# Optimization experiments

Measured on AMD Instinct MI355X. Metric: run time of the kernel, lower is better.

The kernel has to match this reference:

```python
import jax, jax.numpy as jnp
import numpy as np

# Config matching init_kwargs: layer_nb=1 -> stride 16, image 608x608 -> 38x38 grid
B, CIN, H, W = 32, 512, 38, 38
NA, NC = 3, 80
STRIDE = 16.0
ANCHORS = np.array([[30.0, 61.0], [62.0, 45.0], [59.0, 119.0]], dtype=np.float32)


def setup_inputs() -> dict:
    key = jax.random.key(0)
    k1, k2, k3 = jax.random.split(key, 3)
    xin = jax.random.normal(k1, (B, CIN, H, W), dtype=jnp.float32)
    # 1x1 conv weight stored as (out_ch, in_ch); out_ch = NA*(NC+5) = 255
    conv_w = jax.random.normal(k2, (NA * (NC + 5), CIN), dtype=jnp.float32) * 0.02
    conv_b = jax.random.normal(k3, (NA * (NC + 5),), dtype=jnp.float32) * 0.01
    return {"xin": xin, "conv_w": conv_w, "conv_b": conv_b}


def reference(xin, conv_w, conv_b):
    # 1x1 conv == channel GEMM; fuse the NCHW->NHWC permute into the einsum
    fm = jnp.einsum('bchw,oc->bhwo', xin, conv_w) + conv_b  # [B,H,W,255]
    fm = fm.reshape(B, H, W, NA, NC + 5)
    tx, ty, tw, th = fm[..., 0], fm[..., 1], fm[..., 2], fm[..., 3]
    # grid offsets (precomputed via broadcasting instead of per-call numpy rebuild)
    x_off = jnp.arange(W, dtype=fm.dtype)[None, None, :, None]   # broadcast over B,H,NA
    y_off = jnp.arange(H, dtype=fm.dtype)[None, :, None, None]   # broadcast over B,W,NA
    anchors = jnp.asarray(ANCHORS, dtype=fm.dtype)               # [NA,2]
    bx = (jax.nn.sigmoid(tx) + x_off) * STRIDE
    by = (jax.nn.sigmoid(ty) + y_off) * STRIDE
    bw = jnp.exp(tw) * anchors[:, 0]
    bh = jnp.exp(th) * anchors[:, 1]
    boxes = jnp.stack([bx, by, bw, bh], axis=-1)                 # [B,H,W,NA,4]
    # concat decoded boxes with raw objectness + class logits -> [B,H,W,NA,85]
    return jnp.concatenate([boxes, fm[..., 4:]], axis=-1)
```

## Files before the change

kernel.cpp:

```cpp
#include <hip/hip_runtime.h>
#include <cstdint>
#include <cstddef>

#define CIN_K  512
#define WW_    38
#define BHW    1444
#define NOUT   255
#define MTOT   46208

#define BM     32
#define KCH    256
#define ROW_E  260
#define EP_DW  260

typedef __attribute__((ext_vector_type(8))) short  bf16x8;
typedef __attribute__((ext_vector_type(4))) float  floatx4;

static __device__ __forceinline__ unsigned f2bf(float f) {
    unsigned u = __builtin_bit_cast(unsigned, f);
    return (u + 0x7FFFu + ((u >> 16) & 1u)) >> 16;
}

__global__ void conv_w_to_bf16(const float* __restrict__ cw,
                               unsigned short* __restrict__ wb) {
    int tg   = blockIdx.x * 256 + threadIdx.x;
    int base = tg * 8;
    int n    = base >> 9;
    unsigned rr[4] = {0u, 0u, 0u, 0u};
    if (n < NOUT) {
        float4 v0 = *(const float4*)(cw + base);
        float4 v1 = *(const float4*)(cw + base + 4);
        rr[0] = f2bf(v0.x) | (f2bf(v0.y) << 16);
        rr[1] = f2bf(v0.z) | (f2bf(v0.w) << 16);
        rr[2] = f2bf(v1.x) | (f2bf(v1.y) << 16);
        rr[3] = f2bf(v1.z) | (f2bf(v1.w) << 16);
    }
    *(uint4*)(wb + base) = *(uint4*)rr;
}

__global__ __launch_bounds__(256, 6)
void yolo_head(const float* __restrict__ xin,
               const unsigned short* __restrict__ wb,
               const float* __restrict__ cb,
               float* __restrict__ out)
{
    __shared__ unsigned smem[BM * (ROW_E / 2)];
    unsigned short* As = (unsigned short*)smem;

    const int t    = threadIdx.x;
    const int w    = t >> 6;
    const int lane = t & 63;
    const int l15  = lane & 15;
    const int q    = lane >> 4;
    const int m0   = blockIdx.x * BM;

    const int mq4 = (t & 7) * 4;
    const int kq4 = (t >> 3) * 4;
    const int m4  = m0 + mq4;
    const int bi  = m4 / BHW;
    const int hw  = m4 - bi * BHW;
    const float* pb0 = xin + (size_t)bi * (CIN_K * BHW) + hw;

    floatx4 acc[2][4];
#pragma unroll
    for (int i = 0; i < 2; ++i)
#pragma unroll
        for (int j = 0; j < 4; ++j)
            acc[i][j] = (floatx4){0.f, 0.f, 0.f, 0.f};

    const unsigned short* pbw = wb + (size_t)(w * 64 + l15) * CIN_K + q * 8;

#pragma unroll
    for (int ck = 0; ck < 2; ++ck) {
        if (ck) __syncthreads();

#pragma unroll
        for (int it = 0; it < 2; ++it) {
            const int kl = it * 128 + kq4;
            alignas(16) float vv[4][4];
#pragma unroll
            for (int kk = 0; kk < 4; ++kk)
                *(float4*)&vv[kk][0] =
                    *(const float4*)(pb0 + (size_t)(ck * KCH + kl + kk) * BHW);
#pragma unroll
            for (int r = 0; r < 4; ++r) {
                unsigned lo = f2bf(vv[0][r]) | (f2bf(vv[1][r]) << 16);
                unsigned hi = f2bf(vv[2][r]) | (f2bf(vv[3][r]) << 16);
                uint2 pk = make_uint2(lo, hi);
                *(uint2*)(&As[(mq4 + r) * ROW_E + kl]) = pk;
            }
        }
        __syncthreads();

#pragma unroll
        for (int kc = 0; kc < 8; ++kc) {
            bf16x8 bfr[4], af[2];
#pragma unroll
            for (int j = 0; j < 4; ++j) {
                uint4 bv = *(const uint4*)(pbw + (size_t)j * 16 * CIN_K
                                           + ck * KCH + kc * 32);
                bfr[j] = __builtin_bit_cast(bf16x8, bv);
            }
#pragma unroll
            for (int i = 0; i < 2; ++i) {
                int4 av = *(const int4*)(&As[(i * 16 + l15) * ROW_E + kc * 32 + q * 8]);
                af[i] = __builtin_bit_cast(bf16x8, av);
            }
#pragma unroll
            for (int i = 0; i < 2; ++i)
#pragma unroll
                for (int j = 0; j < 4; ++j)
                    acc[i][j] = __builtin_amdgcn_mfma_f32_16x16x32_bf16(
                                    af[i], bfr[j], acc[i][j], 0, 0, 0);
        }
    }

#pragma unroll
    for (int j = 0; j < 4; ++j) {
        int   n    = w * 64 + j * 16 + l15;
        int   nc   = n < NOUT ? n : NOUT - 1;
        int   ai   = nc / 85;
        int   ji   = nc - ai * 85;
        float bias = cb[nc];
        float aw   = (ai == 0) ? 30.f : (ai == 1) ? 62.f : 59.f;
        float ah   = (ai == 0) ? 61.f : (ai == 1) ? 45.f : 119.f;
#pragma unroll
        for (int i = 0; i < 2; ++i)
#pragma unroll
            for (int r = 0; r < 4; ++r) {
                int   md  = m0 + i * 16 + q * 4 + r;
                int   rem = md % BHW;
                int   hh  = rem / WW_;
                float v   = acc[i][j][r] + bias;
                float res;
                if (ji == 0)      res = (1.f / (1.f + __expf(-v)) + (float)(rem - hh * WW_)) * 16.f;
                else if (ji == 1) res = (1.f / (1.f + __expf(-v)) + (float)hh) * 16.f;
                else if (ji == 2) res = __expf(v) * aw;
                else if (ji == 3) res = __expf(v) * ah;
                else              res = v;
                acc[i][j][r] = res;
            }
    }

    float* EP = (float*)smem;
#pragma unroll
    for (int p = 0; p < 2; ++p) {
        __syncthreads();
#pragma unroll
        for (int j = 0; j < 4; ++j)
#pragma unroll
            for (int r = 0; r < 4; ++r)
                EP[(q * 4 + r) * EP_DW + w * 64 + j * 16 + l15] = acc[p][j][r];
        __syncthreads();

        const float* EPb = (const float*)smem + (w * 4) * EP_DW;
        float*       ob  = out + (size_t)(m0 + p * 16 + w * 4) * NOUT;
#pragma unroll
        for (int s2 = 0; s2 < 4; ++s2) {
            int f4 = s2 * 64 + lane;
            if (f4 < 255) {
                int   f = f4 * 4;
                float vs[4];
#pragma unroll
                for (int e = 0; e < 4; ++e) {
                    int fe = f + e;
                    int mr = fe / NOUT;
                    int x  = fe - mr * NOUT;
                    vs[e]  = EPb[mr * EP_DW + x];
                }
                *(float4*)(ob + f) = make_float4(vs[0], vs[1], vs[2], vs[3]);
            }
        }
    }
}

extern "C" void kernel_launch(void* const* d_in, const int* in_sizes, int n_in,
                              void* d_out, int out_size, void* d_ws, size_t ws_size,
                              hipStream_t stream) {
    const float* xin = (const float*)d_in[0];
    const float* cw  = (const float*)d_in[1];
    const float* cb  = (const float*)d_in[2];
    float*       out = (float*)d_out;
    unsigned short* wb = (unsigned short*)d_ws;

    hipLaunchKernelGGL(conv_w_to_bf16, dim3(64), dim3(256), 0, stream, cw, wb);
    hipLaunchKernelGGL(yolo_head, dim3(MTOT / BM), dim3(256), 0, stream,
                       xin, wb, cb, out);
}
```

Measured before the change: 202.4 us.

## Prefetch second K-chunk into registers and remap blocks across XCDs

The kernel issues the global loads for the second 256-channel K chunk into registers before computing on the first chunk, so their latency overlaps the first chunk's MFMA loop. It also remaps block IDs so each XCD handles a contiguous range of M tiles, which is meant to improve L2 locality on the multi-XCD part. The occupancy hint drops from 6 to 4 waves per SIMD to make room for the extra prefetch registers. The trade-off is fewer resident workgroups available to hide memory latency.

```diff
diff --git a/kernel.cpp b/kernel.cpp
--- a/kernel.cpp
+++ b/kernel.cpp
@@ -38,7 +38,7 @@
     *(uint4*)(wb + base) = *(uint4*)rr;
 }
 
-__global__ __launch_bounds__(256, 6)
+__global__ __launch_bounds__(256, 4)
 void yolo_head(const float* __restrict__ xin,
                const unsigned short* __restrict__ wb,
                const float* __restrict__ cb,
@@ -52,7 +52,12 @@
     const int lane = t & 63;
     const int l15  = lane & 15;
     const int q    = lane >> 4;
-    const int m0   = blockIdx.x * BM;
+
+    const int orig = blockIdx.x;
+    const int xcd  = orig & 7;
+    const int rank = orig >> 3;
+    const int wgid = (xcd < 4 ? xcd * 181 : 724 + (xcd - 4) * 180) + rank;
+    const int m0   = wgid * BM;
 
     const int mq4 = (t & 7) * 4;
     const int kq4 = (t >> 3) * 4;
@@ -61,6 +66,30 @@
     const int hw  = m4 - bi * BHW;
     const float* pb0 = xin + (size_t)bi * (CIN_K * BHW) + hw;
 
+    alignas(16) float v0[2][4][4];
+#pragma unroll
+    for (int it = 0; it < 2; ++it)
+#pragma unroll
+        for (int kk = 0; kk < 4; ++kk)
+            *(float4*)&v0[it][kk][0] =
+                *(const float4*)(pb0 + (size_t)(it * 128 + kq4 + kk) * BHW);
+#pragma unroll
+    for (int it = 0; it < 2; ++it)
+#pragma unroll
+        for (int r = 0; r < 4; ++r) {
+            unsigned lo = f2bf(v0[it][0][r]) | (f2bf(v0[it][1][r]) << 16);
+            unsigned hi = f2bf(v0[it][2][r]) | (f2bf(v0[it][3][r]) << 16);
+            *(uint2*)(&As[(mq4 + r) * ROW_E + it * 128 + kq4]) = make_uint2(lo, hi);
+        }
+
+    alignas(16) float v1[2][4][4];
+#pragma unroll
+    for (int it = 0; it < 2; ++it)
+#pragma unroll
+        for (int kk = 0; kk < 4; ++kk)
+            *(float4*)&v1[it][kk][0] =
+                *(const float4*)(pb0 + (size_t)(KCH + it * 128 + kq4 + kk) * BHW);
+
     floatx4 acc[2][4];
 #pragma unroll
     for (int i = 0; i < 2; ++i)
@@ -70,49 +99,62 @@
 
     const unsigned short* pbw = wb + (size_t)(w * 64 + l15) * CIN_K + q * 8;
 
-#pragma unroll
-    for (int ck = 0; ck < 2; ++ck) {
-        if (ck) __syncthreads();
-
-#pragma unroll
-        for (int it = 0; it < 2; ++it) {
-            const int kl = it * 128 + kq4;
-            alignas(16) float vv[4][4];
-#pragma unroll
-            for (int kk = 0; kk < 4; ++kk)
-                *(float4*)&vv[kk][0] =
-                    *(const float4*)(pb0 + (size_t)(ck * KCH + kl + kk) * BHW);
-#pragma unroll
-            for (int r = 0; r < 4; ++r) {
-                unsigned lo = f2bf(vv[0][r]) | (f2bf(vv[1][r]) << 16);
-                unsigned hi = f2bf(vv[2][r]) | (f2bf(vv[3][r]) << 16);
-                uint2 pk = make_uint2(lo, hi);
-                *(uint2*)(&As[(mq4 + r) * ROW_E + kl]) = pk;
-            }
-        }
-        __syncthreads();
-
-#pragma unroll
-        for (int kc = 0; kc < 8; ++kc) {
-            bf16x8 bfr[4], af[2];
-#pragma unroll
-            for (int j = 0; j < 4; ++j) {
-                uint4 bv = *(const uint4*)(pbw + (size_t)j * 16 * CIN_K
-                                           + ck * KCH + kc * 32);
-                bfr[j] = __builtin_bit_cast(bf16x8, bv);
-            }
-#pragma unroll
-            for (int i = 0; i < 2; ++i) {
-                int4 av = *(const int4*)(&As[(i * 16 + l15) * ROW_E + kc * 32 + q * 8]);
-                af[i] = __builtin_bit_cast(bf16x8, av);
-            }
-#pragma unroll
-            for (int i = 0; i < 2; ++i)
-#pragma unroll
-                for (int j = 0; j < 4; ++j)
-                    acc[i][j] = __builtin_amdgcn_mfma_f32_16x16x32_bf16(
-                                    af[i], bfr[j], acc[i][j], 0, 0, 0);
-        }
+    __syncthreads();
+
+#pragma unroll
+    for (int kc = 0; kc < 8; ++kc) {
+        bf16x8 bfr[4], af[2];
+#pragma unroll
+        for (int j = 0; j < 4; ++j) {
+            uint4 bv = *(const uint4*)(pbw + (size_t)j * 16 * CIN_K + kc * 32);
+            bfr[j] = __builtin_bit_cast(bf16x8, bv);
+        }
+#pragma unroll
+        for (int i = 0; i < 2; ++i) {
+            int4 av = *(const int4*)(&As[(i * 16 + l15) * ROW_E + kc * 32 + q * 8]);
+            af[i] = __builtin_bit_cast(bf16x8, av);
+        }
+#pragma unroll
+        for (int i = 0; i < 2; ++i)
+#pragma unroll
+            for (int j = 0; j < 4; ++j)
+                acc[i][j] = __builtin_amdgcn_mfma_f32_16x16x32_bf16(
+                                af[i], bfr[j], acc[i][j], 0, 0, 0);
+    }
+
+    __syncthreads();
+
+#pragma unroll
+    for (int it = 0; it < 2; ++it)
+#pragma unroll
+        for (int r = 0; r < 4; ++r) {
+            unsigned lo = f2bf(v1[it][0][r]) | (f2bf(v1[it][1][r]) << 16);
+            unsigned hi = f2bf(v1[it][2][r]) | (f2bf(v1[it][3][r]) << 16);
+            *(uint2*)(&As[(mq4 + r) * ROW_E + it * 128 + kq4]) = make_uint2(lo, hi);
+        }
+
+    __syncthreads();
+
+#pragma unroll
+    for (int kc = 0; kc < 8; ++kc) {
+        bf16x8 bfr[4], af[2];
+#pragma unroll
+        for (int j = 0; j < 4; ++j) {
+            uint4 bv = *(const uint4*)(pbw + (size_t)j * 16 * CIN_K
+                                       + KCH + kc * 32);
+            bfr[j] = __builtin_bit_cast(bf16x8, bv);
+        }
+#pragma unroll
+        for (int i = 0; i < 2; ++i) {
+            int4 av = *(const int4*)(&As[(i * 16 + l15) * ROW_E + kc * 32 + q * 8]);
+            af[i] = __builtin_bit_cast(bf16x8, av);
+        }
+#pragma unroll
+        for (int i = 0; i < 2; ++i)
+#pragma unroll
+            for (int j = 0; j < 4; ++j)
+                acc[i][j] = __builtin_amdgcn_mfma_f32_16x16x32_bf16(
+                                af[i], bfr[j], acc[i][j], 0, 0, 0);
     }
 
 #pragma unroll
```

Result: faster. 195.7 us (-3.3%).

## Load full K tile up front, remap blocks per XCD, single-pass epilogue

Applied to the files above, without the earlier changes.

The kernel now issues all 64 float4 activation loads for the whole 512-wide K dimension before any compute, instead of two 256-wide chunks separated by a barrier. The LDS tile is doubled so the MFMA loop runs all 16 k-steps without an intermediate sync, and the epilogue stages all 32 rows in one pass. Block IDs are remapped so each XCD handles a contiguous range of M tiles, which should improve L2 locality. It also switches to packed bf16 conversion intrinsics and lowers the occupancy hint from 6 to 4 to make room for the extra registers and LDS, which may reduce latency hiding.

```diff
diff --git a/kernel.cpp b/kernel.cpp
--- a/kernel.cpp
+++ b/kernel.cpp
@@ -1,4 +1,5 @@
 #include <hip/hip_runtime.h>
+#include <hip/hip_bf16.h>
 #include <cstdint>
 #include <cstddef>
 
@@ -9,8 +10,7 @@
 #define MTOT   46208
 
 #define BM     32
-#define KCH    256
-#define ROW_E  260
+#define ROW_E  520
 #define EP_DW  260
 
 typedef __attribute__((ext_vector_type(8))) short  bf16x8;
@@ -19,6 +19,13 @@
 static __device__ __forceinline__ unsigned f2bf(float f) {
     unsigned u = __builtin_bit_cast(unsigned, f);
     return (u + 0x7FFFu + ((u >> 16) & 1u)) >> 16;
+}
+
+static __device__ __forceinline__ unsigned pk2bf(float a, float b) {
+    __hip_bfloat162 h = __float22bfloat162_rn(make_float2(a, b));
+    unsigned r;
+    __builtin_memcpy(&r, &h, 4);
+    return r;
 }
 
 __global__ void conv_w_to_bf16(const float* __restrict__ cw,
@@ -38,7 +45,7 @@
     *(uint4*)(wb + base) = *(uint4*)rr;
 }
 
-__global__ __launch_bounds__(256, 6)
+__global__ __launch_bounds__(256, 4)
 void yolo_head(const float* __restrict__ xin,
                const unsigned short* __restrict__ wb,
                const float* __restrict__ cb,
@@ -52,7 +59,12 @@
     const int lane = t & 63;
     const int l15  = lane & 15;
     const int q    = lane >> 4;
-    const int m0   = blockIdx.x * BM;
+
+    const int orig = blockIdx.x;
+    const int xcd  = orig & 7;
+    const int rank = orig >> 3;
+    const int wgid = (xcd < 4 ? xcd * 181 : 724 + (xcd - 4) * 180) + rank;
+    const int m0   = wgid * BM;
 
     const int mq4 = (t & 7) * 4;
     const int kq4 = (t >> 3) * 4;
@@ -60,6 +72,22 @@
     const int bi  = m4 / BHW;
     const int hw  = m4 - bi * BHW;
     const float* pb0 = xin + (size_t)bi * (CIN_K * BHW) + hw;
+
+    alignas(16) float vv[4][4][4];
+#pragma unroll
+    for (int it = 0; it < 4; ++it)
+#pragma unroll
+        for (int kk = 0; kk < 4; ++kk)
+            *(float4*)&vv[it][kk][0] =
+                *(const float4*)(pb0 + (size_t)(it * 128 + kq4 + kk) * BHW);
+#pragma unroll
+    for (int it = 0; it < 4; ++it)
+#pragma unroll
+        for (int r = 0; r < 4; ++r) {
+            unsigned lo = pk2bf(vv[it][0][r], vv[it][1][r]);
+            unsigned hi = pk2bf(vv[it][2][r], vv[it][3][r]);
+            *(uint2*)(&As[(mq4 + r) * ROW_E + it * 128 + kq4]) = make_uint2(lo, hi);
+        }
 
     floatx4 acc[2][4];
 #pragma unroll
@@ -70,49 +98,27 @@
 
     const unsigned short* pbw = wb + (size_t)(w * 64 + l15) * CIN_K + q * 8;
 
-#pragma unroll
-    for (int ck = 0; ck < 2; ++ck) {
-        if (ck) __syncthreads();
+    __syncthreads();
 
 #pragma unroll
-        for (int it = 0; it < 2; ++it) {
-            const int kl = it * 128 + kq4;
-            alignas(16) float vv[4][4];
+    for (int kc = 0; kc < 16; ++kc) {
+        bf16x8 bfr[4], af[2];
 #pragma unroll
-            for (int kk = 0; kk < 4; ++kk)
-                *(float4*)&vv[kk][0] =
-                    *(const float4*)(pb0 + (size_t)(ck * KCH + kl + kk) * BHW);
+        for (int j = 0; j < 4; ++j) {
+            uint4 bv = *(const uint4*)(pbw + (size_t)j * 16 * CIN_K + kc * 32);
+            bfr[j] = __builtin_bit_cast(bf16x8, bv);
+        }
 #pragma unroll
-            for (int r = 0; r < 4; ++r) {
-                unsigned lo = f2bf(vv[0][r]) | (f2bf(vv[1][r]) << 16);
-                unsigned hi = f2bf(vv[2][r]) | (f2bf(vv[3][r]) << 16);
-                uint2 pk = make_uint2(lo, hi);
-                *(uint2*)(&As[(mq4 + r) * ROW_E + kl]) = pk;
-            }
+        for (int i = 0; i < 2; ++i) {
+            int4 av = *(const int4*)(&As[(i * 16 + l15) * ROW_E + kc * 32 + q * 8]);
+            af[i] = __builtin_bit_cast(bf16x8, av);
         }
-        __syncthreads();
-
 #pragma unroll
-        for (int kc = 0; kc < 8; ++kc) {
-            bf16x8 bfr[4], af[2];
+        for (int i = 0; i < 2; ++i)
 #pragma unroll
-            for (int j = 0; j < 4; ++j) {
-                uint4 bv = *(const uint4*)(pbw + (size_t)j * 16 * CIN_K
-                                           + ck * KCH + kc * 32);
-                bfr[j] = __builtin_bit_cast(bf16x8, bv);
-            }
-#pragma unroll
-            for (int i = 0; i < 2; ++i) {
-                int4 av = *(const int4*)(&As[(i * 16 + l15) * ROW_E + kc * 32 + q * 8]);
-                af[i] = __builtin_bit_cast(bf16x8, av);
-            }
-#pragma unroll
-            for (int i = 0; i < 2; ++i)
-#pragma unroll
-                for (int j = 0; j < 4; ++j)
-                    acc[i][j] = __builtin_amdgcn_mfma_f32_16x16x32_bf16(
-                                    af[i], bfr[j], acc[i][j], 0, 0, 0);
-        }
+            for (int j = 0; j < 4; ++j)
+                acc[i][j] = __builtin_amdgcn_mfma_f32_16x16x32_bf16(
+                                af[i], bfr[j], acc[i][j], 0, 0, 0);
     }
 
 #pragma unroll
@@ -142,23 +148,25 @@
             }
     }
 
+    __syncthreads();
     float* EP = (float*)smem;
 #pragma unroll
-    for (int p = 0; p < 2; ++p) {
-        __syncthreads();
+    for (int i = 0; i < 2; ++i)
 #pragma unroll
         for (int j = 0; j < 4; ++j)
 #pragma unroll
             for (int r = 0; r < 4; ++r)
-                EP[(q * 4 + r) * EP_DW + w * 64 + j * 16 + l15] = acc[p][j][r];
-        __syncthreads();
+                EP[(i * 16 + q * 4 + r) * EP_DW + w * 64 + j * 16 + l15] =
+                    acc[i][j][r];
+    __syncthreads();
 
-        const float* EPb = (const float*)smem + (w * 4) * EP_DW;
-        float*       ob  = out + (size_t)(m0 + p * 16 + w * 4) * NOUT;
+    {
+        const float* EPb = (const float*)smem + (w * 8) * EP_DW;
+        float*       ob  = out + (size_t)(m0 + w * 8) * NOUT;
 #pragma unroll
-        for (int s2 = 0; s2 < 4; ++s2) {
+        for (int s2 = 0; s2 < 8; ++s2) {
             int f4 = s2 * 64 + lane;
-            if (f4 < 255) {
+            if (f4 < 510) {
                 int   f = f4 * 4;
                 float vs[4];
 #pragma unroll
```

New measurement: 196.6 us. 2.9% less time.
